# Performance work log

Hardware: AMD Instinct MI355X
Metric: run time of the kernel (lower is better)

Reference implementation:

```python
import jax, jax.numpy as jnp
import numpy as np

MODEL_DIM = 1024
NUM_HEADS = 16
HEAD_DIM = MODEL_DIM // NUM_HEADS


def setup_inputs() -> dict:
    key = jax.random.key(0)
    ks = jax.random.split(key, 11)
    B, S, D = 2, 2048, MODEL_DIM
    scale = 1.0 / np.sqrt(D)
    inp = {
        "Q": jax.random.normal(ks[0], (B, S, D), jnp.float32),
        "K": jax.random.normal(ks[1], (B, S, D), jnp.float32),
        "V": jax.random.normal(ks[2], (B, S, D), jnp.float32),
        "mask": jnp.tril(jnp.ones((S, S), jnp.int32)),  # causal mask, 0 = blocked
        "Wq": jax.random.normal(ks[3], (D, D), jnp.float32) * scale,
        "bq": jax.random.normal(ks[4], (D,), jnp.float32) * 0.01,
        "Wk": jax.random.normal(ks[5], (D, D), jnp.float32) * scale,
        "bk": jax.random.normal(ks[6], (D,), jnp.float32) * 0.01,
        "Wv": jax.random.normal(ks[7], (D, D), jnp.float32) * scale,
        "bv": jax.random.normal(ks[8], (D,), jnp.float32) * 0.01,
        "Wo": jax.random.normal(ks[9], (D, D), jnp.float32) * scale,
        "bo": jax.random.normal(ks[10], (D,), jnp.float32) * 0.01,
    }
    return inp


def _split_heads(x):
    B, S, D = x.shape
    return x.reshape(B, S, NUM_HEADS, HEAD_DIM).transpose(0, 2, 1, 3)  # [B,H,S,hd]


def reference(Q, K, V, mask, Wq, bq, Wk, bk, Wv, bv, Wo, bo):
    # Linear projections (torch Linear: x @ W^T + b; here W stored as [D,D], use einsum)
    q = _split_heads(Q @ Wq.T + bq)  # [B,H,S,hd]
    k = _split_heads(K @ Wk.T + bk)
    v = _split_heads(V @ Wv.T + bv)
    scores = jnp.einsum("bhqd,bhkd->bhqk", q, k) / jnp.sqrt(jnp.float32(HEAD_DIM))
    # NOTE: source uses masked_fill(mask == 0, -1e-09) -- replicated faithfully
    scores = jnp.where(mask == 0, jnp.float32(-1e-09), scores)
    probs = jax.nn.softmax(scores, axis=-1)
    attn = jnp.einsum("bhqk,bhkd->bhqd", probs, v)  # [B,H,S,hd]
    B, H, S, hd = attn.shape
    out = attn.transpose(0, 2, 1, 3).reshape(B, S, MODEL_DIM)
    return out @ Wo.T + bo
```

## Files before the change

kernel.cpp:

```cpp
#include <hip/hip_runtime.h>
#include <math.h>

#define SEQ 2048
#define DMODEL 1024
#define NHEADS 16
#define HDIM 64
#define BATCH 2
#define MROWS (BATCH*SEQ)
#define BHTOT (BATCH*NHEADS)
#define NKT (SEQ/64)

typedef __attribute__((ext_vector_type(8))) short bf16x8_t;
typedef __attribute__((ext_vector_type(4))) float f32x4_t;
typedef __attribute__((ext_vector_type(16))) float f32x16_t;
typedef unsigned short u16;
typedef unsigned int u32;

__device__ __forceinline__ u16 f2bf(float x) {
    u32 u = __float_as_uint(x);
    return (u16)((u + 0x7FFFu + ((u >> 16) & 1u)) >> 16);
}
__device__ __forceinline__ float bf2f(u16 h) {
    return __uint_as_float(((u32)h) << 16);
}
__device__ __forceinline__ int swz(int row, int colbyte) {
    return colbyte ^ ((row & 7) << 4);
}
__device__ __forceinline__ u32 cvtpk(float a, float b) {
    u32 r;
    asm("v_cvt_pk_bf16_f32 %0, %1, %2" : "=v"(r) : "v"(a), "v"(b));
    return r;
}
__device__ __forceinline__ void plswap(u32& a, u32& b) {
    asm("v_permlane32_swap_b32 %0, %1" : "+v"(a), "+v"(b));
}
__device__ __forceinline__ float bfhi_lo(u32 w) { return __uint_as_float(w << 16); }
__device__ __forceinline__ float bfhi_hi(u32 w) { return __uint_as_float(w & 0xFFFF0000u); }

__global__ void split_w4(const float* __restrict__ w0, const float* __restrict__ w1,
                         const float* __restrict__ w2, const float* __restrict__ w3,
                         u16* __restrict__ hi, u16* __restrict__ lo, int n4) {
    const float* src[4] = {w0, w1, w2, w3};
    const float* in = src[blockIdx.y];
    u16* h = hi + (size_t)blockIdx.y * DMODEL * DMODEL;
    u16* l = lo + (size_t)blockIdx.y * DMODEL * DMODEL;
    int idx = blockIdx.x * blockDim.x + threadIdx.x;
    int stride = gridDim.x * blockDim.x;
    for (int i = idx; i < n4; i += stride) {
        float4 v = ((const float4*)in)[i];
        ushort4 hh, ll;
        hh.x = f2bf(v.x); ll.x = f2bf(v.x - bf2f(hh.x));
        hh.y = f2bf(v.y); ll.y = f2bf(v.y - bf2f(hh.y));
        hh.z = f2bf(v.z); ll.z = f2bf(v.z - bf2f(hh.z));
        hh.w = f2bf(v.w); ll.w = f2bf(v.w - bf2f(hh.w));
        ((ushort4*)h)[i] = hh;
        ((ushort4*)l)[i] = ll;
    }
}

__global__ __launch_bounds__(256)
void gemm_qkv(const float* __restrict__ Qf, const float* __restrict__ Kf,
              const float* __restrict__ Vf,
              const u16* __restrict__ whi, const u16* __restrict__ wlo,
              const float* __restrict__ bq, const float* __restrict__ bk,
              const float* __restrict__ bv,
              u16* __restrict__ q_hi, u16* __restrict__ q_lo,
              u16* __restrict__ k_hi, u16* __restrict__ k_lo,
              u16* __restrict__ vt_hi, u16* __restrict__ vt_lo) {
    const int K = 1024, N = 1024;
    const size_t WSZ = (size_t)DMODEL * DMODEL;
    __shared__ u16 As_h[128 * 40];
    __shared__ u16 As_l[128 * 40];
    __shared__ u16 Ws_h[128 * 40];
    __shared__ u16 Ws_l[128 * 40];

    const int z = blockIdx.z;
    const float* Afp = (z == 0) ? Qf : (z == 1) ? Kf : Vf;
    const u16* Whi = whi + (size_t)z * WSZ;
    const u16* Wlo = wlo + (size_t)z * WSZ;
    const float* bias = (z == 0) ? bq : (z == 1) ? bk : bv;
    const float oscale = (z == 0) ? 0.125f : 1.f;

    const int tid = threadIdx.x;
    const int lane = tid & 63, w = tid >> 6;
    const int wr = w >> 1, wc = w & 1;
    const int m0 = blockIdx.y * 128, n0 = blockIdx.x * 128;
    const int rb = lane & 15, ko = (lane >> 4) * 8;

    f32x4_t acc[4][4];
    #pragma unroll
    for (int i = 0; i < 4; ++i)
        #pragma unroll
        for (int j = 0; j < 4; ++j)
            acc[i][j] = (f32x4_t){0.f, 0.f, 0.f, 0.f};

    for (int k0 = 0; k0 < K; k0 += 32) {
        #pragma unroll
        for (int s = 0; s < 2; ++s) {
            int c = tid + s * 256;
            int r = c >> 2, q = c & 3;
            size_t ga = (size_t)(m0 + r) * K + k0 + q * 8;
            size_t gw = (size_t)(n0 + r) * K + k0 + q * 8;
            int la = r * 40 + q * 8;
            float4 a0 = *(const float4*)(Afp + ga);
            float4 a1 = *(const float4*)(Afp + ga + 4);
            u32 h0 = cvtpk(a0.x, a0.y), h1 = cvtpk(a0.z, a0.w);
            u32 h2 = cvtpk(a1.x, a1.y), h3 = cvtpk(a1.z, a1.w);
            u32 l0 = cvtpk(a0.x - bfhi_lo(h0), a0.y - bfhi_hi(h0));
            u32 l1 = cvtpk(a0.z - bfhi_lo(h1), a0.w - bfhi_hi(h1));
            u32 l2 = cvtpk(a1.x - bfhi_lo(h2), a1.y - bfhi_hi(h2));
            u32 l3 = cvtpk(a1.z - bfhi_lo(h3), a1.w - bfhi_hi(h3));
            *(uint4*)&As_h[la] = (uint4){h0, h1, h2, h3};
            *(uint4*)&As_l[la] = (uint4){l0, l1, l2, l3};
            *(uint4*)&Ws_h[la] = *(const uint4*)&Whi[gw];
            *(uint4*)&Ws_l[la] = *(const uint4*)&Wlo[gw];
        }
        __syncthreads();

        bf16x8_t ah[4], al[4];
        #pragma unroll
        for (int i = 0; i < 4; ++i) {
            int ra = wr * 64 + i * 16 + rb;
            ah[i] = *(const bf16x8_t*)&As_h[ra * 40 + ko];
            al[i] = *(const bf16x8_t*)&As_l[ra * 40 + ko];
        }
        #pragma unroll
        for (int j = 0; j < 4; ++j) {
            int rw = wc * 64 + j * 16 + rb;
            bf16x8_t wh = *(const bf16x8_t*)&Ws_h[rw * 40 + ko];
            bf16x8_t wl = *(const bf16x8_t*)&Ws_l[rw * 40 + ko];
            #pragma unroll
            for (int i = 0; i < 4; ++i) {
                acc[i][j] = __builtin_amdgcn_mfma_f32_16x16x32_bf16(ah[i], wh, acc[i][j], 0, 0, 0);
                acc[i][j] = __builtin_amdgcn_mfma_f32_16x16x32_bf16(ah[i], wl, acc[i][j], 0, 0, 0);
                acc[i][j] = __builtin_amdgcn_mfma_f32_16x16x32_bf16(al[i], wh, acc[i][j], 0, 0, 0);
            }
        }
        __syncthreads();
    }

    if (z == 2) {
        #pragma unroll
        for (int i = 0; i < 4; ++i)
            #pragma unroll
            for (int j = 0; j < 4; ++j) {
                int mb = m0 + wr * 64 + i * 16 + (lane >> 4) * 4;
                int n = n0 + wc * 64 + j * 16 + rb;
                int bb = mb >> 11, s0 = mb & (SEQ - 1);
                int hh = n >> 6, dd = n & 63;
                size_t idx = (((size_t)(bb * 16 + hh) * 64) + dd) * SEQ + s0;
                float bn = bias[n];
                ushort4 h4, l4;
                float v0 = acc[i][j][0] + bn;
                float v1 = acc[i][j][1] + bn;
                float v2 = acc[i][j][2] + bn;
                float v3 = acc[i][j][3] + bn;
                h4.x = f2bf(v0); l4.x = f2bf(v0 - bf2f(h4.x));
                h4.y = f2bf(v1); l4.y = f2bf(v1 - bf2f(h4.y));
                h4.z = f2bf(v2); l4.z = f2bf(v2 - bf2f(h4.z));
                h4.w = f2bf(v3); l4.w = f2bf(v3 - bf2f(h4.w));
                *(ushort4*)&vt_hi[idx] = h4;
                *(ushort4*)&vt_lo[idx] = l4;
            }
    } else {
        u16* Ch = (z == 0) ? q_hi : k_hi;
        u16* Cl = (z == 0) ? q_lo : k_lo;
        #pragma unroll
        for (int i = 0; i < 4; ++i)
            #pragma unroll
            for (int j = 0; j < 4; ++j)
                #pragma unroll
                for (int r = 0; r < 4; ++r) {
                    int m = m0 + wr * 64 + i * 16 + (lane >> 4) * 4 + r;
                    int n = n0 + wc * 64 + j * 16 + rb;
                    float v = (acc[i][j][r] + bias[n]) * oscale;
                    int bb = m >> 11, s = m & (SEQ - 1);
                    int hh = n >> 6, dd = n & 63;
                    size_t idx = (((size_t)(bb * 16 + hh) * SEQ) + s) * 64 + dd;
                    u16 t = f2bf(v);
                    Ch[idx] = t;
                    Cl[idx] = f2bf(v - bf2f(t));
                }
    }
}

__global__ __launch_bounds__(256)
void gemm_out(const u16* __restrict__ Ahi, const u16* __restrict__ Alo,
              const u16* __restrict__ Whi, const u16* __restrict__ Wlo,
              const float* __restrict__ bias, float* __restrict__ C) {
    const int K = 1024, N = 1024;
    __shared__ u16 As_h[64 * 40];
    __shared__ u16 As_l[64 * 40];
    __shared__ u16 Ws_h[128 * 40];
    __shared__ u16 Ws_l[128 * 40];

    const int tid = threadIdx.x;
    const int lane = tid & 63, w = tid >> 6;
    const int m0 = blockIdx.y * 64, n0 = blockIdx.x * 128;
    const int rb = lane & 15, ko = (lane >> 4) * 8;

    f32x4_t acc[4][2];
    #pragma unroll
    for (int i = 0; i < 4; ++i)
        #pragma unroll
        for (int j = 0; j < 2; ++j)
            acc[i][j] = (f32x4_t){0.f, 0.f, 0.f, 0.f};

    for (int k0 = 0; k0 < K; k0 += 32) {
        {
            int r = tid >> 2, q = tid & 3;
            size_t ga = (size_t)(m0 + r) * K + k0 + q * 8;
            int la = r * 40 + q * 8;
            *(uint4*)&As_h[la] = *(const uint4*)&Ahi[ga];
            *(uint4*)&As_l[la] = *(const uint4*)&Alo[ga];
        }
        #pragma unroll
        for (int s = 0; s < 2; ++s) {
            int c = tid + s * 256;
            int r = c >> 2, q = c & 3;
            size_t gw = (size_t)(n0 + r) * K + k0 + q * 8;
            int la = r * 40 + q * 8;
            *(uint4*)&Ws_h[la] = *(const uint4*)&Whi[gw];
            *(uint4*)&Ws_l[la] = *(const uint4*)&Wlo[gw];
        }
        __syncthreads();

        bf16x8_t ah[4], al[4];
        #pragma unroll
        for (int i = 0; i < 4; ++i) {
            int ra = i * 16 + rb;
            ah[i] = *(const bf16x8_t*)&As_h[ra * 40 + ko];
            al[i] = *(const bf16x8_t*)&As_l[ra * 40 + ko];
        }
        #pragma unroll
        for (int j = 0; j < 2; ++j) {
            int rw = w * 32 + j * 16 + rb;
            bf16x8_t wh = *(const bf16x8_t*)&Ws_h[rw * 40 + ko];
            bf16x8_t wl = *(const bf16x8_t*)&Ws_l[rw * 40 + ko];
            #pragma unroll
            for (int i = 0; i < 4; ++i) {
                acc[i][j] = __builtin_amdgcn_mfma_f32_16x16x32_bf16(ah[i], wh, acc[i][j], 0, 0, 0);
                acc[i][j] = __builtin_amdgcn_mfma_f32_16x16x32_bf16(ah[i], wl, acc[i][j], 0, 0, 0);
                acc[i][j] = __builtin_amdgcn_mfma_f32_16x16x32_bf16(al[i], wh, acc[i][j], 0, 0, 0);
            }
        }
        __syncthreads();
    }

    #pragma unroll
    for (int i = 0; i < 4; ++i)
        #pragma unroll
        for (int j = 0; j < 2; ++j)
            #pragma unroll
            for (int r = 0; r < 4; ++r) {
                int m = m0 + i * 16 + (lane >> 4) * 4 + r;
                int n = n0 + w * 32 + j * 16 + rb;
                C[(size_t)m * N + n] = acc[i][j][r] + bias[n];
            }
}

__global__ void vcolsum(const u16* __restrict__ vth, const u16* __restrict__ vtl,
                        float* __restrict__ cs) {
    int kt = blockIdx.x, bh = blockIdx.y, d = threadIdx.x;
    const u16* ph = vth + ((size_t)bh * 64 + d) * SEQ + kt * 64;
    const u16* pl = vtl + ((size_t)bh * 64 + d) * SEQ + kt * 64;
    float s = 0.f;
    #pragma unroll 16
    for (int j = 0; j < 64; ++j) s += bf2f(ph[j]) + bf2f(pl[j]);
    cs[((size_t)bh * NKT + kt) * 64 + d] = s;
}

__global__ void suffix_scan(const float* __restrict__ cs, float* __restrict__ suf) {
    int bh = blockIdx.x, d = threadIdx.x;
    float acc = 0.f;
    for (int kt = NKT - 1; kt >= 0; --kt) {
        acc += cs[((size_t)bh * NKT + kt) * 64 + d];
        suf[((size_t)bh * NKT + kt) * 64 + d] = acc;
    }
}

__global__ __launch_bounds__(256)
void attn_mfma(const u16* __restrict__ qh_g, const u16* __restrict__ ql_g,
               const u16* __restrict__ kh_g, const u16* __restrict__ kl_g,
               const u16* __restrict__ vth_g, const u16* __restrict__ vtl_g,
               const float* __restrict__ suf,
               u16* __restrict__ ahi, u16* __restrict__ alo) {
    __shared__ alignas(16) u16 Kh[4096], Kl[4096];
    __shared__ alignas(16) u16 Vh[4096], Vl[4096];

    const int tid = threadIdx.x;
    const int lane = tid & 63, w = tid >> 6;
    const int q31 = lane & 31, g2 = lane >> 5;
    const int sidx = blockIdx.x >> 5;
    const int stripe = (sidx < 8) ? (15 - sidx) : (sidx - 8);
    const int bh = blockIdx.x & 31;
    const int b = bh >> 4, h = bh & 15;
    const int qb0 = stripe << 7;
    const int dt_w = 2 * stripe + (w >> 1);
    const int nt_blk = 2 * stripe + 2;
    const int qrow = qb0 + w * 32 + q31;

    bf16x8_t qfh[4], qfl[4];
    {
        const u16* qp = qh_g + ((size_t)bh * SEQ + qrow) * 64;
        const u16* qp2 = ql_g + ((size_t)bh * SEQ + qrow) * 64;
        #pragma unroll
        for (int ks = 0; ks < 4; ++ks) {
            qfh[ks] = *(const bf16x8_t*)(qp + ks * 16 + g2 * 8);
            qfl[ks] = *(const bf16x8_t*)(qp2 + ks * 16 + g2 * 8);
        }
    }

    f32x16_t o[2];
    #pragma unroll
    for (int dt = 0; dt < 2; ++dt)
        #pragma unroll
        for (int r = 0; r < 16; ++r) o[dt][r] = 0.f;
    float mrow = -1e30f, lrow = 0.f;

    const u16* khb = kh_g + (size_t)bh * SEQ * 64;
    const u16* klb = kl_g + (size_t)bh * SEQ * 64;
    const u16* vhb = vth_g + (size_t)bh * 64 * SEQ;
    const u16* vlb = vtl_g + (size_t)bh * 64 * SEQ;

    for (int kt = 0; kt < nt_blk; ++kt) {
        if (kt) __syncthreads();
        #pragma unroll
        for (int s = 0; s < 2; ++s) {
            int gg = tid + s * 256;
            int row = gg >> 3, dg = gg & 7;
            int off = row * 128 + swz(row, dg * 16);
            *(uint4*)((char*)Kh + off) = *(const uint4*)(khb + (size_t)(kt * 64 + row) * 64 + dg * 8);
            *(uint4*)((char*)Kl + off) = *(const uint4*)(klb + (size_t)(kt * 64 + row) * 64 + dg * 8);
            *(uint4*)((char*)Vh + off) = *(const uint4*)(vhb + (size_t)row * SEQ + kt * 64 + dg * 8);
            *(uint4*)((char*)Vl + off) = *(const uint4*)(vlb + (size_t)row * SEQ + kt * 64 + dg * 8);
        }
        __syncthreads();
        if (kt > dt_w) continue;

        f32x16_t st[2];
        #pragma unroll
        for (int jt = 0; jt < 2; ++jt)
            #pragma unroll
            for (int r = 0; r < 16; ++r) st[jt][r] = 0.f;
        #pragma unroll
        for (int ks = 0; ks < 4; ++ks)
            #pragma unroll
            for (int jt = 0; jt < 2; ++jt) {
                int row = jt * 32 + q31;
                int off = row * 128 + swz(row, ks * 32 + g2 * 16);
                bf16x8_t kh8 = *(const bf16x8_t*)((char*)Kh + off);
                bf16x8_t kl8 = *(const bf16x8_t*)((char*)Kl + off);
                st[jt] = __builtin_amdgcn_mfma_f32_32x32x16_bf16(kh8, qfh[ks], st[jt], 0, 0, 0);
                st[jt] = __builtin_amdgcn_mfma_f32_32x32x16_bf16(kh8, qfl[ks], st[jt], 0, 0, 0);
                st[jt] = __builtin_amdgcn_mfma_f32_32x32x16_bf16(kl8, qfh[ks], st[jt], 0, 0, 0);
            }

        if (kt == dt_w) {
            #pragma unroll
            for (int jt = 0; jt < 2; ++jt)
                #pragma unroll
                for (int r = 0; r < 16; ++r) {
                    int j = kt * 64 + jt * 32 + (r & 3) + 8 * (r >> 2) + 4 * g2;
                    if (j > qrow) st[jt][r] = -1e-9f;
                }
        }

        float mx = -1e30f;
        #pragma unroll
        for (int jt = 0; jt < 2; ++jt)
            #pragma unroll
            for (int r = 0; r < 16; ++r) mx = fmaxf(mx, st[jt][r]);
        mx = fmaxf(mx, __shfl_xor(mx, 32));
        float nm = fmaxf(mrow, mx);
        float alpha = __expf(mrow - nm);
        mrow = nm;
        float rs = 0.f;
        #pragma unroll
        for (int jt = 0; jt < 2; ++jt)
            #pragma unroll
            for (int r = 0; r < 16; ++r) {
                float p = __expf(st[jt][r] - nm);
                st[jt][r] = p;
                rs += p;
            }
        rs += __shfl_xor(rs, 32);
        lrow = lrow * alpha + rs;
        #pragma unroll
        for (int dt = 0; dt < 2; ++dt)
            #pragma unroll
            for (int r = 0; r < 16; ++r) o[dt][r] *= alpha;

        bf16x8_t pbh[4], pbl[4];
        #pragma unroll
        for (int jt = 0; jt < 2; ++jt) {
            u32 hq[8], lq[8];
            #pragma unroll
            for (int p2 = 0; p2 < 8; ++p2) {
                float s0 = st[jt][p2 * 2], s1 = st[jt][p2 * 2 + 1];
                u32 hk = cvtpk(s0, s1);
                hq[p2] = hk;
                float l0 = s0 - __uint_as_float(hk << 16);
                float l1 = s1 - __uint_as_float(hk & 0xFFFF0000u);
                lq[p2] = cvtpk(l0, l1);
            }
            plswap(hq[0], hq[2]); plswap(hq[1], hq[3]);
            plswap(hq[4], hq[6]); plswap(hq[5], hq[7]);
            plswap(lq[0], lq[2]); plswap(lq[1], lq[3]);
            plswap(lq[4], lq[6]); plswap(lq[5], lq[7]);
            uint4 t;
            t = (uint4){hq[0], hq[1], hq[2], hq[3]};
            pbh[2 * jt] = *(bf16x8_t*)&t;
            t = (uint4){hq[4], hq[5], hq[6], hq[7]};
            pbh[2 * jt + 1] = *(bf16x8_t*)&t;
            t = (uint4){lq[0], lq[1], lq[2], lq[3]};
            pbl[2 * jt] = *(bf16x8_t*)&t;
            t = (uint4){lq[4], lq[5], lq[6], lq[7]};
            pbl[2 * jt + 1] = *(bf16x8_t*)&t;
        }

        #pragma unroll
        for (int ks = 0; ks < 4; ++ks)
            #pragma unroll
            for (int dt = 0; dt < 2; ++dt) {
                int row = dt * 32 + q31;
                int off = row * 128 + swz(row, ks * 32 + g2 * 16);
                bf16x8_t vh8 = *(const bf16x8_t*)((char*)Vh + off);
                bf16x8_t vl8 = *(const bf16x8_t*)((char*)Vl + off);
                o[dt] = __builtin_amdgcn_mfma_f32_32x32x16_bf16(vh8, pbh[ks], o[dt], 0, 0, 0);
                o[dt] = __builtin_amdgcn_mfma_f32_32x32x16_bf16(vh8, pbl[ks], o[dt], 0, 0, 0);
                o[dt] = __builtin_amdgcn_mfma_f32_32x32x16_bf16(vl8, pbh[ks], o[dt], 0, 0, 0);
            }
    }

    const int nt_w = dt_w + 1;
    const int nfull = NKT - nt_w;
    if (nfull > 0) {
        float mm = fmaxf(mrow, -1e-9f);
        float al2 = __expf(mrow - mm);
        float ee = __expf(-1e-9f - mm);
        lrow = lrow * al2 + ee * (64.f * (float)nfull);
        const float* sufp = suf + ((size_t)bh * NKT + nt_w) * 64;
        #pragma unroll
        for (int dt = 0; dt < 2; ++dt)
            #pragma unroll
            for (int qq = 0; qq < 4; ++qq) {
                int d0 = dt * 32 + qq * 8 + g2 * 4;
                float4 sf = *(const float4*)(sufp + d0);
                o[dt][qq * 4 + 0] = o[dt][qq * 4 + 0] * al2 + ee * sf.x;
                o[dt][qq * 4 + 1] = o[dt][qq * 4 + 1] * al2 + ee * sf.y;
                o[dt][qq * 4 + 2] = o[dt][qq * 4 + 2] * al2 + ee * sf.z;
                o[dt][qq * 4 + 3] = o[dt][qq * 4 + 3] * al2 + ee * sf.w;
            }
    }

    float inv = 1.f / lrow;
    size_t rowg = (size_t)b * SEQ + qrow;
    #pragma unroll
    for (int dt = 0; dt < 2; ++dt)
        #pragma unroll
        for (int qq = 0; qq < 4; ++qq) {
            int d0 = dt * 32 + qq * 8 + g2 * 4;
            ushort4 h4, l4;
            float v0 = o[dt][qq * 4 + 0] * inv;
            float v1 = o[dt][qq * 4 + 1] * inv;
            float v2 = o[dt][qq * 4 + 2] * inv;
            float v3 = o[dt][qq * 4 + 3] * inv;
            h4.x = f2bf(v0); l4.x = f2bf(v0 - bf2f(h4.x));
            h4.y = f2bf(v1); l4.y = f2bf(v1 - bf2f(h4.y));
            h4.z = f2bf(v2); l4.z = f2bf(v2 - bf2f(h4.z));
            h4.w = f2bf(v3); l4.w = f2bf(v3 - bf2f(h4.w));
            size_t col = (size_t)h * 64 + d0;
            *(ushort4*)&ahi[rowg * DMODEL + col] = h4;
            *(ushort4*)&alo[rowg * DMODEL + col] = l4;
        }
}

extern "C" void kernel_launch(void* const* d_in, const int* in_sizes, int n_in,
                              void* d_out, int out_size, void* d_ws, size_t ws_size,
                              hipStream_t stream) {
    const float* Q   = (const float*)d_in[0];
    const float* K   = (const float*)d_in[1];
    const float* V   = (const float*)d_in[2];
    const float* Wq  = (const float*)d_in[4];
    const float* bq  = (const float*)d_in[5];
    const float* Wk  = (const float*)d_in[6];
    const float* bk  = (const float*)d_in[7];
    const float* Wv  = (const float*)d_in[8];
    const float* bv  = (const float*)d_in[9];
    const float* Wo  = (const float*)d_in[10];
    const float* bo  = (const float*)d_in[11];
    float* out = (float*)d_out;

    float* ws = (float*)d_ws;
    const size_t HEADSZ = (size_t)BHTOT * SEQ * HDIM;
    const size_t WSZ = (size_t)DMODEL * DMODEL;
    float* cs_ws  = ws;
    float* suf_ws = ws + 65536;
    u16* base  = (u16*)(ws + 131072);
    u16* q_hi  = base;
    u16* q_lo  = base + HEADSZ;
    u16* k_hi  = base + 2 * HEADSZ;
    u16* k_lo  = base + 3 * HEADSZ;
    u16* vt_hi = base + 4 * HEADSZ;
    u16* vt_lo = base + 5 * HEADSZ;
    u16* in_hi = base + 6 * HEADSZ;
    u16* in_lo = base + 7 * HEADSZ;
    u16* w_hi  = base + 8 * HEADSZ;
    u16* w_lo  = w_hi + 4 * WSZ;

    const int W_N4 = (int)(WSZ / 4);
    dim3 sblk(256);
    dim3 gblk(256);
    dim3 gout(DMODEL / 128, MROWS / 64);
    dim3 gqkv(DMODEL / 128, MROWS / 128, 3);

    split_w4<<<dim3(512, 4), sblk, 0, stream>>>(Wq, Wk, Wv, Wo, w_hi, w_lo, W_N4);

    gemm_qkv<<<gqkv, gblk, 0, stream>>>(Q, K, V, w_hi, w_lo, bq, bk, bv,
                                        q_hi, q_lo, k_hi, k_lo, vt_hi, vt_lo);

    vcolsum<<<dim3(NKT, BHTOT), dim3(64), 0, stream>>>(vt_hi, vt_lo, cs_ws);
    suffix_scan<<<dim3(BHTOT), dim3(64), 0, stream>>>(cs_ws, suf_ws);

    attn_mfma<<<dim3(16 * BHTOT), gblk, 0, stream>>>(q_hi, q_lo, k_hi, k_lo,
                                                     vt_hi, vt_lo, suf_ws,
                                                     in_hi, in_lo);

    gemm_out<<<gout, gblk, 0, stream>>>(in_hi, in_lo, w_hi + 3 * WSZ,
                                        w_lo + 3 * WSZ, bo, out);
}
```

Measured before the change: 240.7 us.

## Halve QKV GEMM row tile and merge V column-sum with suffix scan

The QKV projection GEMM now uses a 64x128 tile with each of four waves owning a 32-column slice, instead of a 128x128 tile split two by two. This doubles the grid to 1536 blocks, improving occupancy and wave balance across the CUs at the cost of less reuse of each A and W tile. The separate vcolsum and suffix_scan kernels are merged into one vsuffix kernel, saving a launch and an intermediate buffer. The merged kernel runs only 32 blocks of 64 threads, each reading its whole V row serially, so that step has much less parallelism.

```diff
diff --git a/kernel.cpp b/kernel.cpp
--- a/kernel.cpp
+++ b/kernel.cpp
@@ -69,8 +69,8 @@
               u16* __restrict__ vt_hi, u16* __restrict__ vt_lo) {
     const int K = 1024, N = 1024;
     const size_t WSZ = (size_t)DMODEL * DMODEL;
-    __shared__ u16 As_h[128 * 40];
-    __shared__ u16 As_l[128 * 40];
+    __shared__ u16 As_h[64 * 40];
+    __shared__ u16 As_l[64 * 40];
     __shared__ u16 Ws_h[128 * 40];
     __shared__ u16 Ws_l[128 * 40];
 
@@ -83,24 +83,20 @@
 
     const int tid = threadIdx.x;
     const int lane = tid & 63, w = tid >> 6;
-    const int wr = w >> 1, wc = w & 1;
-    const int m0 = blockIdx.y * 128, n0 = blockIdx.x * 128;
+    const int m0 = blockIdx.y * 64, n0 = blockIdx.x * 128;
     const int rb = lane & 15, ko = (lane >> 4) * 8;
 
-    f32x4_t acc[4][4];
+    f32x4_t acc[4][2];
     #pragma unroll
     for (int i = 0; i < 4; ++i)
         #pragma unroll
-        for (int j = 0; j < 4; ++j)
+        for (int j = 0; j < 2; ++j)
             acc[i][j] = (f32x4_t){0.f, 0.f, 0.f, 0.f};
 
     for (int k0 = 0; k0 < K; k0 += 32) {
-        #pragma unroll
-        for (int s = 0; s < 2; ++s) {
-            int c = tid + s * 256;
-            int r = c >> 2, q = c & 3;
+        {
+            int r = tid >> 2, q = tid & 3;
             size_t ga = (size_t)(m0 + r) * K + k0 + q * 8;
-            size_t gw = (size_t)(n0 + r) * K + k0 + q * 8;
             int la = r * 40 + q * 8;
             float4 a0 = *(const float4*)(Afp + ga);
             float4 a1 = *(const float4*)(Afp + ga + 4);
@@ -112,6 +108,13 @@
             u32 l3 = cvtpk(a1.z - bfhi_lo(h3), a1.w - bfhi_hi(h3));
             *(uint4*)&As_h[la] = (uint4){h0, h1, h2, h3};
             *(uint4*)&As_l[la] = (uint4){l0, l1, l2, l3};
+        }
+        #pragma unroll
+        for (int s = 0; s < 2; ++s) {
+            int c = tid + s * 256;
+            int r = c >> 2, q = c & 3;
+            size_t gw = (size_t)(n0 + r) * K + k0 + q * 8;
+            int la = r * 40 + q * 8;
             *(uint4*)&Ws_h[la] = *(const uint4*)&Whi[gw];
             *(uint4*)&Ws_l[la] = *(const uint4*)&Wlo[gw];
         }
@@ -120,13 +123,13 @@
         bf16x8_t ah[4], al[4];
         #pragma unroll
         for (int i = 0; i < 4; ++i) {
-            int ra = wr * 64 + i * 16 + rb;
+            int ra = i * 16 + rb;
             ah[i] = *(const bf16x8_t*)&As_h[ra * 40 + ko];
             al[i] = *(const bf16x8_t*)&As_l[ra * 40 + ko];
         }
         #pragma unroll
-        for (int j = 0; j < 4; ++j) {
-            int rw = wc * 64 + j * 16 + rb;
+        for (int j = 0; j < 2; ++j) {
+            int rw = w * 32 + j * 16 + rb;
             bf16x8_t wh = *(const bf16x8_t*)&Ws_h[rw * 40 + ko];
             bf16x8_t wl = *(const bf16x8_t*)&Ws_l[rw * 40 + ko];
             #pragma unroll
@@ -143,9 +146,9 @@
         #pragma unroll
         for (int i = 0; i < 4; ++i)
             #pragma unroll
-            for (int j = 0; j < 4; ++j) {
-                int mb = m0 + wr * 64 + i * 16 + (lane >> 4) * 4;
-                int n = n0 + wc * 64 + j * 16 + rb;
+            for (int j = 0; j < 2; ++j) {
+                int mb = m0 + i * 16 + (lane >> 4) * 4;
+                int n = n0 + w * 32 + j * 16 + rb;
                 int bb = mb >> 11, s0 = mb & (SEQ - 1);
                 int hh = n >> 6, dd = n & 63;
                 size_t idx = (((size_t)(bb * 16 + hh) * 64) + dd) * SEQ + s0;
@@ -168,11 +171,11 @@
         #pragma unroll
         for (int i = 0; i < 4; ++i)
             #pragma unroll
-            for (int j = 0; j < 4; ++j)
+            for (int j = 0; j < 2; ++j)
                 #pragma unroll
                 for (int r = 0; r < 4; ++r) {
-                    int m = m0 + wr * 64 + i * 16 + (lane >> 4) * 4 + r;
-                    int n = n0 + wc * 64 + j * 16 + rb;
+                    int m = m0 + i * 16 + (lane >> 4) * 4 + r;
+                    int n = n0 + w * 32 + j * 16 + rb;
                     float v = (acc[i][j][r] + bias[n]) * oscale;
                     int bb = m >> 11, s = m & (SEQ - 1);
                     int hh = n >> 6, dd = n & 63;
@@ -259,22 +262,18 @@
             }
 }
 
-__global__ void vcolsum(const u16* __restrict__ vth, const u16* __restrict__ vtl,
-                        float* __restrict__ cs) {
-    int kt = blockIdx.x, bh = blockIdx.y, d = threadIdx.x;
-    const u16* ph = vth + ((size_t)bh * 64 + d) * SEQ + kt * 64;
-    const u16* pl = vtl + ((size_t)bh * 64 + d) * SEQ + kt * 64;
-    float s = 0.f;
-    #pragma unroll 16
-    for (int j = 0; j < 64; ++j) s += bf2f(ph[j]) + bf2f(pl[j]);
-    cs[((size_t)bh * NKT + kt) * 64 + d] = s;
-}
-
-__global__ void suffix_scan(const float* __restrict__ cs, float* __restrict__ suf) {
+__global__ void vsuffix(const u16* __restrict__ vth, const u16* __restrict__ vtl,
+                        float* __restrict__ suf) {
     int bh = blockIdx.x, d = threadIdx.x;
+    const u16* ph = vth + ((size_t)bh * 64 + d) * SEQ;
+    const u16* pl = vtl + ((size_t)bh * 64 + d) * SEQ;
     float acc = 0.f;
     for (int kt = NKT - 1; kt >= 0; --kt) {
-        acc += cs[((size_t)bh * NKT + kt) * 64 + d];
+        float s = 0.f;
+        #pragma unroll 16
+        for (int j = 0; j < 64; ++j)
+            s += bf2f(ph[kt * 64 + j]) + bf2f(pl[kt * 64 + j]);
+        acc += s;
         suf[((size_t)bh * NKT + kt) * 64 + d] = acc;
     }
 }
@@ -495,8 +494,7 @@
     float* ws = (float*)d_ws;
     const size_t HEADSZ = (size_t)BHTOT * SEQ * HDIM;
     const size_t WSZ = (size_t)DMODEL * DMODEL;
-    float* cs_ws  = ws;
-    float* suf_ws = ws + 65536;
+    float* suf_ws = ws;
     u16* base  = (u16*)(ws + 131072);
     u16* q_hi  = base;
     u16* q_lo  = base + HEADSZ;
@@ -513,15 +511,14 @@
     dim3 sblk(256);
     dim3 gblk(256);
     dim3 gout(DMODEL / 128, MROWS / 64);
-    dim3 gqkv(DMODEL / 128, MROWS / 128, 3);
+    dim3 gqkv(DMODEL / 128, MROWS / 64, 3);
 
     split_w4<<<dim3(512, 4), sblk, 0, stream>>>(Wq, Wk, Wv, Wo, w_hi, w_lo, W_N4);
 
     gemm_qkv<<<gqkv, gblk, 0, stream>>>(Q, K, V, w_hi, w_lo, bq, bk, bv,
                                         q_hi, q_lo, k_hi, k_lo, vt_hi, vt_lo);
 
-    vcolsum<<<dim3(NKT, BHTOT), dim3(64), 0, stream>>>(vt_hi, vt_lo, cs_ws);
-    suffix_scan<<<dim3(BHTOT), dim3(64), 0, stream>>>(cs_ws, suf_ws);
+    vsuffix<<<dim3(BHTOT), dim3(64), 0, stream>>>(vt_hi, vt_lo, suf_ws);
 
     attn_mfma<<<dim3(16 * BHTOT), gblk, 0, stream>>>(q_hi, q_lo, k_hi, k_lo,
                                                      vt_hi, vt_lo, suf_ws,
```

New measurement: 269.6 us. +12.0%, slower.
